# Optimization experiments

Hardware: AMD Instinct MI355X
Metric: run time of the kernel (lower is better)

Reference implementation:

```python
import jax, jax.numpy as jnp
import numpy as np

B, N, M = 128, 256, 1024
EPS = 1e-16
NORM_EPS = 1e-8  # torch cosine_similarity denominator clamp


def setup_inputs() -> dict:
    key = jax.random.key(0)
    ks = jax.random.split(key, 9)
    return {
        "memory": jax.random.normal(ks[0], (B, N, M), jnp.float32),
        "k": jax.random.normal(ks[1], (B, M), jnp.float32),
        "beta": jax.random.uniform(ks[2], (B, 1), jnp.float32),
        "g": jax.random.uniform(ks[3], (B, 1), jnp.float32),
        "s": jax.random.uniform(ks[4], (B, 3), jnp.float32),
        "gamma": jax.random.uniform(ks[5], (B, 1), jnp.float32),
        "w_prev": jax.random.uniform(ks[6], (B, N), jnp.float32),
        "e": jax.random.uniform(ks[7], (B, M), jnp.float32),
        "a": jax.random.normal(ks[8], (B, M), jnp.float32),
    }


def reference(memory, k, beta, g, s, gamma, w_prev, e, a):
    # --- _similarity: cosine similarity + softmax over N rows ---
    mem_e = memory + EPS              # (B, N, M)
    k_e = k + EPS                     # (B, M)
    dot = jnp.einsum("bnm,bm->bn", mem_e, k_e)
    mnorm = jnp.maximum(jnp.linalg.norm(mem_e, axis=-1), NORM_EPS)      # (B, N)
    knorm = jnp.maximum(jnp.linalg.norm(k_e, axis=-1), NORM_EPS)        # (B,)
    cos = dot / (mnorm * knorm[:, None])
    w_c = jax.nn.softmax(beta * cos, axis=-1)                           # (B, N)

    # --- _interpolate with previous weighting ---
    w_g = g * w_c + (1.0 - g) * w_prev                                  # (B, N)

    # --- _shift: circular convolution with 3-tap kernel s ---
    # result[m] = s0*w[m-1] + s1*w[m] + s2*w[m+1]  (circular, matches _convolve)
    w_t = (s[:, 0:1] * jnp.roll(w_g, 1, axis=1)
           + s[:, 1:2] * w_g
           + s[:, 2:3] * jnp.roll(w_g, -1, axis=1))                     # (B, N)

    # --- _sharpen ---
    w_pow = w_t ** gamma
    w = w_pow / (jnp.sum(w_pow, axis=1, keepdims=True) + EPS)           # (B, N)

    # --- write: batched outer-product erase/add (fused, no per-batch loop) ---
    erase = jnp.einsum("bn,bm->bnm", w, e)                              # (B, N, M)
    add = jnp.einsum("bn,bm->bnm", w, a)                                # (B, N, M)
    new_memory = memory * (1.0 - erase) + add

    # --- read ---
    read = jnp.einsum("bn,bnm->bm", w, new_memory)                      # (B, M)

    return read, new_memory, w
```

## Files before the change

### kernel.cpp

```cpp
#include <hip/hip_runtime.h>

#define B_ 128
#define N_ 256
#define M_ 1024
#define EPS_ 1e-16f
#define NORM_EPS_ 1e-8f

#define SPLIT_ 8
#define NSUB_ (N_ / SPLIT_)

__device__ __forceinline__ float wave_reduce_sum(float v) {
#pragma unroll
    for (int off = 32; off; off >>= 1) v += __shfl_xor(v, off, 64);
    return v;
}

__device__ __forceinline__ float wave_reduce_max(float v) {
#pragma unroll
    for (int off = 32; off; off >>= 1) v = fmaxf(v, __shfl_xor(v, off, 64));
    return v;
}

__global__ void sim_kernel(const float* __restrict__ memory,
                           const float* __restrict__ k,
                           float* __restrict__ dot_out,
                           float* __restrict__ mnorm2_out) {
    const int wave = threadIdx.x >> 6;
    const int lane = threadIdx.x & 63;
    const int row  = blockIdx.x * 4 + wave;
    const int b    = row >> 8;

    const float4* __restrict__ mrow = (const float4*)(memory + (size_t)row * M_);
    const float4* __restrict__ krow = (const float4*)(k + (size_t)b * M_);

    float dacc = 0.f, nacc = 0.f;
#pragma unroll
    for (int it = 0; it < 4; ++it) {
        const int idx = it * 64 + lane;
        float4 mv = mrow[idx];
        float4 kv = krow[idx];
        float m0 = mv.x + EPS_, m1 = mv.y + EPS_, m2 = mv.z + EPS_, m3 = mv.w + EPS_;
        float k0 = kv.x + EPS_, k1 = kv.y + EPS_, k2 = kv.z + EPS_, k3 = kv.w + EPS_;
        dacc += m0 * k0 + m1 * k1 + m2 * k2 + m3 * k3;
        nacc += m0 * m0 + m1 * m1 + m2 * m2 + m3 * m3;
    }
    dacc = wave_reduce_sum(dacc);
    nacc = wave_reduce_sum(nacc);
    if (lane == 0) {
        dot_out[row]    = dacc;
        mnorm2_out[row] = nacc;
    }
}

__global__ void weight_kernel(const float* __restrict__ k,
                              const float* __restrict__ beta,
                              const float* __restrict__ g,
                              const float* __restrict__ s,
                              const float* __restrict__ gamma,
                              const float* __restrict__ w_prev,
                              const float* __restrict__ dot_in,
                              const float* __restrict__ mnorm2_in,
                              float* __restrict__ w_out,
                              float* __restrict__ read_out) {
    const int b    = blockIdx.x;
    const int tid  = threadIdx.x;
    const int lane = tid & 63;
    const int wave = tid >> 6;

    __shared__ float red[4];
    __shared__ float s_wg[N_];

    float4 z = {0.f, 0.f, 0.f, 0.f};
    ((float4*)(read_out + (size_t)b * M_))[tid] = z;

    float4 kv = ((const float4*)(k + (size_t)b * M_))[tid];
    float k0 = kv.x + EPS_, k1 = kv.y + EPS_, k2 = kv.z + EPS_, k3 = kv.w + EPS_;
    float kk = k0 * k0 + k1 * k1 + k2 * k2 + k3 * k3;
    kk = wave_reduce_sum(kk);
    if (lane == 0) red[wave] = kk;
    __syncthreads();
    float knorm = fmaxf(sqrtf(red[0] + red[1] + red[2] + red[3]), NORM_EPS_);
    __syncthreads();

    const int n = tid;
    const float mnorm = fmaxf(sqrtf(mnorm2_in[(size_t)b * N_ + n]), NORM_EPS_);
    const float cosv  = dot_in[(size_t)b * N_ + n] / (mnorm * knorm);
    const float x     = beta[b] * cosv;

    float mx = wave_reduce_max(x);
    if (lane == 0) red[wave] = mx;
    __syncthreads();
    mx = fmaxf(fmaxf(red[0], red[1]), fmaxf(red[2], red[3]));
    __syncthreads();
    float ex = __expf(x - mx);
    float es = wave_reduce_sum(ex);
    if (lane == 0) red[wave] = es;
    __syncthreads();
    es = red[0] + red[1] + red[2] + red[3];
    __syncthreads();
    const float w_c = ex / es;

    const float gb  = g[b];
    const float w_g = gb * w_c + (1.f - gb) * w_prev[(size_t)b * N_ + n];
    s_wg[n] = w_g;
    __syncthreads();

    const float s0 = s[b * 3 + 0], s1 = s[b * 3 + 1], s2 = s[b * 3 + 2];
    const float w_t = s0 * s_wg[(n + N_ - 1) & (N_ - 1)]
                    + s1 * s_wg[n]
                    + s2 * s_wg[(n + 1) & (N_ - 1)];

    const float w_pow = powf(w_t, gamma[b]);
    float ps = wave_reduce_sum(w_pow);
    if (lane == 0) red[wave] = ps;
    __syncthreads();
    ps = red[0] + red[1] + red[2] + red[3];

    w_out[(size_t)b * N_ + n] = w_pow / (ps + EPS_);
}

__global__ void write_read_kernel(const float* __restrict__ memory,
                                  const float* __restrict__ e,
                                  const float* __restrict__ a,
                                  const float* __restrict__ w,
                                  float* __restrict__ newmem_out,
                                  float* __restrict__ read_out) {
    const int b    = blockIdx.x / SPLIT_;
    const int part = blockIdx.x % SPLIT_;
    const int tid  = threadIdx.x;

    __shared__ float s_w[NSUB_];
    if (tid < NSUB_) s_w[tid] = w[(size_t)b * N_ + part * NSUB_ + tid];
    __syncthreads();

    const float4 ev = ((const float4*)(e + (size_t)b * M_))[tid];
    const float4 av = ((const float4*)(a + (size_t)b * M_))[tid];

    const size_t base = (size_t)b * N_ * M_;
    float4 racc = {0.f, 0.f, 0.f, 0.f};

#pragma unroll 4
    for (int j = 0; j < NSUB_; ++j) {
        const int n = part * NSUB_ + j;
        const float4 mv = ((const float4*)(memory + base + (size_t)n * M_))[tid];
        const float wn = s_w[j];
        float4 nv;
        nv.x = mv.x * (1.f - wn * ev.x) + wn * av.x;
        nv.y = mv.y * (1.f - wn * ev.y) + wn * av.y;
        nv.z = mv.z * (1.f - wn * ev.z) + wn * av.z;
        nv.w = mv.w * (1.f - wn * ev.w) + wn * av.w;
        ((float4*)(newmem_out + base + (size_t)n * M_))[tid] = nv;
        racc.x += wn * nv.x;
        racc.y += wn * nv.y;
        racc.z += wn * nv.z;
        racc.w += wn * nv.w;
    }

    float* rrow = read_out + (size_t)b * M_ + tid * 4;
    atomicAdd(rrow + 0, racc.x);
    atomicAdd(rrow + 1, racc.y);
    atomicAdd(rrow + 2, racc.z);
    atomicAdd(rrow + 3, racc.w);
}

extern "C" void kernel_launch(void* const* d_in, const int* in_sizes, int n_in,
                              void* d_out, int out_size, void* d_ws, size_t ws_size,
                              hipStream_t stream) {
    (void)in_sizes; (void)n_in; (void)out_size; (void)ws_size;

    const float* memory = (const float*)d_in[0];
    const float* k      = (const float*)d_in[1];
    const float* beta   = (const float*)d_in[2];
    const float* g      = (const float*)d_in[3];
    const float* s      = (const float*)d_in[4];
    const float* gamma  = (const float*)d_in[5];
    const float* w_prev = (const float*)d_in[6];
    const float* e      = (const float*)d_in[7];
    const float* a      = (const float*)d_in[8];

    float* out        = (float*)d_out;
    float* read_out   = out;
    float* newmem_out = out + (size_t)B_ * M_;
    float* w_out      = newmem_out + (size_t)B_ * N_ * M_;

    float* ws        = (float*)d_ws;
    float* dot_ws    = ws;
    float* mnorm2_ws = ws + (size_t)B_ * N_;

    sim_kernel<<<(B_ * N_) / 4, 256, 0, stream>>>(memory, k, dot_ws, mnorm2_ws);
    weight_kernel<<<B_, 256, 0, stream>>>(k, beta, g, s, gamma, w_prev,
                                          dot_ws, mnorm2_ws, w_out, read_out);
    write_read_kernel<<<B_ * SPLIT_, 256, 0, stream>>>(memory, e, a, w_out,
                                                       newmem_out, read_out);
}
```

Measured before the change: 273.8 us.

## Fuse three kernels into one cooperative kernel with grid syncs and nontemporal memory access

Replaces the three separate launches (similarity, weighting, write/read) with a single cooperative kernel of 1024 blocks that uses grid-wide syncs between phases. Each block handles the same 32 memory rows in the similarity phase and in the write phase, so the second pass over memory may hit in cache. The write phase now uses nontemporal loads and stores. The cost is two grid barriers, and only 128 blocks do work during the weighting phase while the rest sit idle.

```diff
diff --git a/kernel.cpp b/kernel.cpp
--- a/kernel.cpp
+++ b/kernel.cpp
@@ -1,4 +1,7 @@
 #include <hip/hip_runtime.h>
+#include <hip/hip_cooperative_groups.h>
+
+namespace cg = cooperative_groups;
 
 #define B_ 128
 #define N_ 256
@@ -6,8 +9,12 @@
 #define EPS_ 1e-16f
 #define NORM_EPS_ 1e-8f
 
+#define GRID_ 1024
+#define ROWS_PER_BLOCK_ 32
 #define SPLIT_ 8
-#define NSUB_ (N_ / SPLIT_)
+#define NSUB_ 32
+
+typedef float f32x4 __attribute__((ext_vector_type(4)));
 
 __device__ __forceinline__ float wave_reduce_sum(float v) {
 #pragma unroll
@@ -21,146 +28,150 @@
     return v;
 }
 
-__global__ void sim_kernel(const float* __restrict__ memory,
-                           const float* __restrict__ k,
-                           float* __restrict__ dot_out,
-                           float* __restrict__ mnorm2_out) {
-    const int wave = threadIdx.x >> 6;
-    const int lane = threadIdx.x & 63;
-    const int row  = blockIdx.x * 4 + wave;
-    const int b    = row >> 8;
-
-    const float4* __restrict__ mrow = (const float4*)(memory + (size_t)row * M_);
-    const float4* __restrict__ krow = (const float4*)(k + (size_t)b * M_);
-
-    float dacc = 0.f, nacc = 0.f;
-#pragma unroll
-    for (int it = 0; it < 4; ++it) {
-        const int idx = it * 64 + lane;
-        float4 mv = mrow[idx];
-        float4 kv = krow[idx];
-        float m0 = mv.x + EPS_, m1 = mv.y + EPS_, m2 = mv.z + EPS_, m3 = mv.w + EPS_;
-        float k0 = kv.x + EPS_, k1 = kv.y + EPS_, k2 = kv.z + EPS_, k3 = kv.w + EPS_;
-        dacc += m0 * k0 + m1 * k1 + m2 * k2 + m3 * k3;
-        nacc += m0 * m0 + m1 * m1 + m2 * m2 + m3 * m3;
-    }
-    dacc = wave_reduce_sum(dacc);
-    nacc = wave_reduce_sum(nacc);
-    if (lane == 0) {
-        dot_out[row]    = dacc;
-        mnorm2_out[row] = nacc;
-    }
-}
-
-__global__ void weight_kernel(const float* __restrict__ k,
-                              const float* __restrict__ beta,
-                              const float* __restrict__ g,
-                              const float* __restrict__ s,
-                              const float* __restrict__ gamma,
-                              const float* __restrict__ w_prev,
-                              const float* __restrict__ dot_in,
-                              const float* __restrict__ mnorm2_in,
-                              float* __restrict__ w_out,
-                              float* __restrict__ read_out) {
-    const int b    = blockIdx.x;
+__global__ void __launch_bounds__(256, 4)
+ntm_fused_kernel(const float* __restrict__ memory,
+                 const float* __restrict__ k,
+                 const float* __restrict__ beta,
+                 const float* __restrict__ g,
+                 const float* __restrict__ s,
+                 const float* __restrict__ gamma,
+                 const float* __restrict__ w_prev,
+                 const float* __restrict__ e,
+                 const float* __restrict__ a,
+                 float* __restrict__ read_out,
+                 float* __restrict__ newmem_out,
+                 float* __restrict__ w_out,
+                 float* __restrict__ dot_ws,
+                 float* __restrict__ mnorm2_ws) {
+    cg::grid_group grid = cg::this_grid();
+
     const int tid  = threadIdx.x;
     const int lane = tid & 63;
     const int wave = tid >> 6;
+    const int blk  = blockIdx.x;
 
     __shared__ float red[4];
     __shared__ float s_wg[N_];
-
-    float4 z = {0.f, 0.f, 0.f, 0.f};
-    ((float4*)(read_out + (size_t)b * M_))[tid] = z;
-
-    float4 kv = ((const float4*)(k + (size_t)b * M_))[tid];
-    float k0 = kv.x + EPS_, k1 = kv.y + EPS_, k2 = kv.z + EPS_, k3 = kv.w + EPS_;
-    float kk = k0 * k0 + k1 * k1 + k2 * k2 + k3 * k3;
-    kk = wave_reduce_sum(kk);
-    if (lane == 0) red[wave] = kk;
-    __syncthreads();
-    float knorm = fmaxf(sqrtf(red[0] + red[1] + red[2] + red[3]), NORM_EPS_);
-    __syncthreads();
-
-    const int n = tid;
-    const float mnorm = fmaxf(sqrtf(mnorm2_in[(size_t)b * N_ + n]), NORM_EPS_);
-    const float cosv  = dot_in[(size_t)b * N_ + n] / (mnorm * knorm);
-    const float x     = beta[b] * cosv;
-
-    float mx = wave_reduce_max(x);
-    if (lane == 0) red[wave] = mx;
-    __syncthreads();
-    mx = fmaxf(fmaxf(red[0], red[1]), fmaxf(red[2], red[3]));
-    __syncthreads();
-    float ex = __expf(x - mx);
-    float es = wave_reduce_sum(ex);
-    if (lane == 0) red[wave] = es;
-    __syncthreads();
-    es = red[0] + red[1] + red[2] + red[3];
-    __syncthreads();
-    const float w_c = ex / es;
-
-    const float gb  = g[b];
-    const float w_g = gb * w_c + (1.f - gb) * w_prev[(size_t)b * N_ + n];
-    s_wg[n] = w_g;
-    __syncthreads();
-
-    const float s0 = s[b * 3 + 0], s1 = s[b * 3 + 1], s2 = s[b * 3 + 2];
-    const float w_t = s0 * s_wg[(n + N_ - 1) & (N_ - 1)]
-                    + s1 * s_wg[n]
-                    + s2 * s_wg[(n + 1) & (N_ - 1)];
-
-    const float w_pow = powf(w_t, gamma[b]);
-    float ps = wave_reduce_sum(w_pow);
-    if (lane == 0) red[wave] = ps;
-    __syncthreads();
-    ps = red[0] + red[1] + red[2] + red[3];
-
-    w_out[(size_t)b * N_ + n] = w_pow / (ps + EPS_);
-}
-
-__global__ void write_read_kernel(const float* __restrict__ memory,
-                                  const float* __restrict__ e,
-                                  const float* __restrict__ a,
-                                  const float* __restrict__ w,
-                                  float* __restrict__ newmem_out,
-                                  float* __restrict__ read_out) {
-    const int b    = blockIdx.x / SPLIT_;
-    const int part = blockIdx.x % SPLIT_;
-    const int tid  = threadIdx.x;
-
     __shared__ float s_w[NSUB_];
-    if (tid < NSUB_) s_w[tid] = w[(size_t)b * N_ + part * NSUB_ + tid];
-    __syncthreads();
-
-    const float4 ev = ((const float4*)(e + (size_t)b * M_))[tid];
-    const float4 av = ((const float4*)(a + (size_t)b * M_))[tid];
-
-    const size_t base = (size_t)b * N_ * M_;
-    float4 racc = {0.f, 0.f, 0.f, 0.f};
+
+    if (tid < 128) read_out[blk * 128 + tid] = 0.f;
+
+    {
+        const int b = blk >> 3;
+        const f32x4* __restrict__ krow = (const f32x4*)(k + (size_t)b * M_);
+        for (int j = 0; j < 8; ++j) {
+            const int row = blk * ROWS_PER_BLOCK_ + wave * 8 + j;
+            const f32x4* __restrict__ mrow = (const f32x4*)(memory + (size_t)row * M_);
+            float dacc = 0.f, nacc = 0.f;
+#pragma unroll
+            for (int it = 0; it < 4; ++it) {
+                const int idx = it * 64 + lane;
+                f32x4 mv = mrow[idx];
+                f32x4 kv = krow[idx];
+                float m0 = mv.x + EPS_, m1 = mv.y + EPS_, m2 = mv.z + EPS_, m3 = mv.w + EPS_;
+                float c0 = kv.x + EPS_, c1 = kv.y + EPS_, c2 = kv.z + EPS_, c3 = kv.w + EPS_;
+                dacc += m0 * c0 + m1 * c1 + m2 * c2 + m3 * c3;
+                nacc += m0 * m0 + m1 * m1 + m2 * m2 + m3 * m3;
+            }
+            dacc = wave_reduce_sum(dacc);
+            nacc = wave_reduce_sum(nacc);
+            if (lane == 0) {
+                dot_ws[row]    = dacc;
+                mnorm2_ws[row] = nacc;
+            }
+        }
+    }
+
+    grid.sync();
+
+    if (blk < B_) {
+        const int b = blk;
+        const int n = tid;
+
+        f32x4 kv = ((const f32x4*)(k + (size_t)b * M_))[tid];
+        float k0 = kv.x + EPS_, k1 = kv.y + EPS_, k2 = kv.z + EPS_, k3 = kv.w + EPS_;
+        float kk = k0 * k0 + k1 * k1 + k2 * k2 + k3 * k3;
+        kk = wave_reduce_sum(kk);
+        if (lane == 0) red[wave] = kk;
+        __syncthreads();
+        const float knorm = fmaxf(sqrtf(red[0] + red[1] + red[2] + red[3]), NORM_EPS_);
+        __syncthreads();
+
+        const float mnorm = fmaxf(sqrtf(mnorm2_ws[(size_t)b * N_ + n]), NORM_EPS_);
+        const float cosv  = dot_ws[(size_t)b * N_ + n] / (mnorm * knorm);
+        const float x     = beta[b] * cosv;
+
+        float mx = wave_reduce_max(x);
+        if (lane == 0) red[wave] = mx;
+        __syncthreads();
+        mx = fmaxf(fmaxf(red[0], red[1]), fmaxf(red[2], red[3]));
+        __syncthreads();
+        const float ex = __expf(x - mx);
+        float es = wave_reduce_sum(ex);
+        if (lane == 0) red[wave] = es;
+        __syncthreads();
+        es = red[0] + red[1] + red[2] + red[3];
+        __syncthreads();
+        const float w_c = ex / es;
+
+        const float gb  = g[b];
+        const float w_g = gb * w_c + (1.f - gb) * w_prev[(size_t)b * N_ + n];
+        s_wg[n] = w_g;
+        __syncthreads();
+
+        const float s0 = s[b * 3 + 0], s1 = s[b * 3 + 1], s2 = s[b * 3 + 2];
+        const float w_t = s0 * s_wg[(n + N_ - 1) & (N_ - 1)]
+                        + s1 * s_wg[n]
+                        + s2 * s_wg[(n + 1) & (N_ - 1)];
+
+        const float w_pow = powf(w_t, gamma[b]);
+        float ps = wave_reduce_sum(w_pow);
+        if (lane == 0) red[wave] = ps;
+        __syncthreads();
+        ps = red[0] + red[1] + red[2] + red[3];
+
+        w_out[(size_t)b * N_ + n] = w_pow / (ps + EPS_);
+    }
+
+    grid.sync();
+
+    {
+        const int b    = blk >> 3;
+        const int part = blk & 7;
+
+        if (tid < NSUB_) s_w[tid] = w_out[(size_t)b * N_ + part * NSUB_ + tid];
+        __syncthreads();
+
+        const f32x4 ev = ((const f32x4*)(e + (size_t)b * M_))[tid];
+        const f32x4 av = ((const f32x4*)(a + (size_t)b * M_))[tid];
+
+        const size_t base = (size_t)b * N_ * M_;
+        f32x4 racc = {0.f, 0.f, 0.f, 0.f};
 
 #pragma unroll 4
-    for (int j = 0; j < NSUB_; ++j) {
-        const int n = part * NSUB_ + j;
-        const float4 mv = ((const float4*)(memory + base + (size_t)n * M_))[tid];
-        const float wn = s_w[j];
-        float4 nv;
-        nv.x = mv.x * (1.f - wn * ev.x) + wn * av.x;
-        nv.y = mv.y * (1.f - wn * ev.y) + wn * av.y;
-        nv.z = mv.z * (1.f - wn * ev.z) + wn * av.z;
-        nv.w = mv.w * (1.f - wn * ev.w) + wn * av.w;
-        ((float4*)(newmem_out + base + (size_t)n * M_))[tid] = nv;
-        racc.x += wn * nv.x;
-        racc.y += wn * nv.y;
-        racc.z += wn * nv.z;
-        racc.w += wn * nv.w;
+        for (int j = 0; j < NSUB_; ++j) {
+            const int n = part * NSUB_ + j;
+            const f32x4* mrow = (const f32x4*)(memory + base + (size_t)n * M_);
+            const f32x4 mv = __builtin_nontemporal_load(mrow + tid);
+            const float wn = s_w[j];
+            f32x4 nv;
+            nv.x = mv.x * (1.f - wn * ev.x) + wn * av.x;
+            nv.y = mv.y * (1.f - wn * ev.y) + wn * av.y;
+            nv.z = mv.z * (1.f - wn * ev.z) + wn * av.z;
+            nv.w = mv.w * (1.f - wn * ev.w) + wn * av.w;
+            __builtin_nontemporal_store(nv, (f32x4*)(newmem_out + base + (size_t)n * M_) + tid);
+            racc.x += wn * nv.x;
+            racc.y += wn * nv.y;
+            racc.z += wn * nv.z;
+            racc.w += wn * nv.w;
+        }
+
+        float* rrow = read_out + (size_t)b * M_ + tid * 4;
+        atomicAdd(rrow + 0, racc.x);
+        atomicAdd(rrow + 1, racc.y);
+        atomicAdd(rrow + 2, racc.z);
+        atomicAdd(rrow + 3, racc.w);
     }
-
-    float* rrow = read_out + (size_t)b * M_ + tid * 4;
-    atomicAdd(rrow + 0, racc.x);
-    atomicAdd(rrow + 1, racc.y);
-    atomicAdd(rrow + 2, racc.z);
-    atomicAdd(rrow + 3, racc.w);
 }
 
 extern "C" void kernel_launch(void* const* d_in, const int* in_sizes, int n_in,
@@ -187,9 +198,12 @@
     float* dot_ws    = ws;
     float* mnorm2_ws = ws + (size_t)B_ * N_;
 
-    sim_kernel<<<(B_ * N_) / 4, 256, 0, stream>>>(memory, k, dot_ws, mnorm2_ws);
-    weight_kernel<<<B_, 256, 0, stream>>>(k, beta, g, s, gamma, w_prev,
-                                          dot_ws, mnorm2_ws, w_out, read_out);
-    write_read_kernel<<<B_ * SPLIT_, 256, 0, stream>>>(memory, e, a, w_out,
-                                                       newmem_out, read_out);
-}
+    void* args[] = {
+        (void*)&memory, (void*)&k, (void*)&beta, (void*)&g, (void*)&s,
+        (void*)&gamma, (void*)&w_prev, (void*)&e, (void*)&a,
+        (void*)&read_out, (void*)&newmem_out, (void*)&w_out,
+        (void*)&dot_ws, (void*)&mnorm2_ws
+    };
+    hipLaunchCooperativeKernel((const void*)ntm_fused_kernel,
+                               dim3(GRID_), dim3(256), args, 0, stream);
+}
```

After: 500.3 us. 82.7% more time.
